# Kernel tuning notes

Measured on AMD Instinct MI355X. Metric: run time of the kernel, lower is better.

Reference implementation:

```python
import jax, jax.numpy as jnp
import numpy as np

B, T, TWO_H = 64, 512, 1024  # batch, prev decoding steps, 2*hidden_dim


def setup_inputs() -> dict:
    key = jax.random.key(0)
    k1, k2, k3 = jax.random.split(key, 3)
    h_d_t = jax.random.normal(k1, (B, TWO_H), dtype=jnp.float32)
    prev_h_dec = jax.random.normal(k2, (B, T, TWO_H), dtype=jnp.float32)
    # nn.Bilinear(2H, 2H, attn_dim=1) weight, trunc_norm_init_std ~ 1e-4 typical
    W = jax.random.normal(k3, (1, TWO_H, TWO_H), dtype=jnp.float32) * 1e-4
    return {"h_d_t": h_d_t, "prev_h_dec": prev_h_dec, "W": W}


def reference(h_d_t, prev_h_dec, W):
    # Bilinear score: s[b,t] = h_d_t[b] @ W[0] @ prev_h_dec[b,t]
    q = jnp.einsum('bd,de->be', h_d_t, W[0])          # (B, 2H) -- one small GEMM
    attn_score = jnp.einsum('be,bte->bt', q, prev_h_dec)  # (B, T)
    alpha_t = jax.nn.softmax(attn_score, axis=1)      # (B, T)
    ct_d = jnp.einsum('bt,btd->bd', alpha_t, prev_h_dec)  # (B, 2H)
    new_prev = jnp.concatenate([prev_h_dec, h_d_t[:, None, :]], axis=1)  # (B, T+1, 2H)
    return (ct_d, new_prev)
```

## Files before the change

kernel.cpp:

```cpp
#include <hip/hip_runtime.h>
#include <math.h>

#define BB    64
#define TT    512
#define TWOH  1024
#define TC    16
#define NCHUNK (TT / TC)
#define KSPLIT 4
#define NP_STRIDE ((TT + 1) * TWOH)

typedef float vfloat4 __attribute__((ext_vector_type(4)));


__global__ __launch_bounds__(256) void k_qgemm(const float* __restrict__ h,
                                               const float* __restrict__ W,
                                               float* __restrict__ qpart) {
    const int tid = threadIdx.x;
    const int e   = blockIdx.x * 256 + tid;
    const int b   = blockIdx.y;
    const int k   = blockIdx.z;
    const int d0  = k * (TWOH / KSPLIT);

    __shared__ float sh[TWOH / KSPLIT];
    sh[tid] = h[b * TWOH + d0 + tid];
    __syncthreads();

    const float* __restrict__ Wp = W + (size_t)d0 * TWOH + e;
    float acc = 0.f;
    #pragma unroll 16
    for (int d = 0; d < TWOH / KSPLIT; ++d)
        acc = fmaf(sh[d], Wp[(size_t)d * TWOH], acc);

    qpart[((size_t)k * BB + b) * TWOH + e] = acc;
}

__global__ __launch_bounds__(256, 4) void k_scores_ct(const float* __restrict__ prev,
                                                      const float* __restrict__ qpart,
                                                      float* __restrict__ out_np,
                                                      float* __restrict__ ws_m,
                                                      float* __restrict__ ws_l,
                                                      float* __restrict__ ws_ct) {
    const int c   = blockIdx.x;
    const int b   = blockIdx.y;
    const int t0  = c * TC;
    const int tid = threadIdx.x;
    const int lane = tid & 63;
    const int wid  = tid >> 6;

    __shared__ float s_part[TC][4];
    __shared__ float s_score[TC];

    const vfloat4* __restrict__ prow =
        (const vfloat4*)(prev + (size_t)b * TT * TWOH + (size_t)t0 * TWOH) + tid;
    vfloat4* __restrict__ nprow =
        (vfloat4*)(out_np + (size_t)b * NP_STRIDE + (size_t)t0 * TWOH) + tid;

    const vfloat4* __restrict__ qp = (const vfloat4*)qpart;
    vfloat4 q4 = qp[((size_t)0 * BB + b) * 256 + tid]
               + qp[((size_t)1 * BB + b) * 256 + tid]
               + qp[((size_t)2 * BB + b) * 256 + tid]
               + qp[((size_t)3 * BB + b) * 256 + tid];

    vfloat4 pv[TC];
    #pragma unroll
    for (int t = 0; t < TC; ++t)
        pv[t] = prow[t * 256];

    #pragma unroll
    for (int t = 0; t < TC; ++t) {
        float pd = pv[t].x * q4.x + pv[t].y * q4.y + pv[t].z * q4.z + pv[t].w * q4.w;
        #pragma unroll
        for (int off = 32; off > 0; off >>= 1)
            pd += __shfl_xor(pd, off, 64);
        if (lane == 0) s_part[t][wid] = pd;
    }
    __syncthreads();
    if (tid < TC)
        s_score[tid] = s_part[tid][0] + s_part[tid][1] + s_part[tid][2] + s_part[tid][3];
    __syncthreads();

    float m = -INFINITY;
    #pragma unroll
    for (int t = 0; t < TC; ++t) m = fmaxf(m, s_score[t]);
    float l = 0.f;
    vfloat4 ct = (vfloat4)(0.f);
    #pragma unroll
    for (int t = 0; t < TC; ++t) {
        const float w = __expf(s_score[t] - m);
        l += w;
        ct.x = fmaf(w, pv[t].x, ct.x);
        ct.y = fmaf(w, pv[t].y, ct.y);
        ct.z = fmaf(w, pv[t].z, ct.z);
        ct.w = fmaf(w, pv[t].w, ct.w);
    }
    ((vfloat4*)(ws_ct + ((size_t)b * NCHUNK + c) * TWOH))[tid] = ct;
    if (tid == 0) {
        ws_m[b * NCHUNK + c] = m;
        ws_l[b * NCHUNK + c] = l;
    }

    #pragma unroll
    for (int t = 0; t < TC; ++t)
        nprow[t * 256] = pv[t];
}

__global__ __launch_bounds__(256) void k_finalize(const float* __restrict__ h,
                                                  const float* __restrict__ ws_m,
                                                  const float* __restrict__ ws_l,
                                                  const float* __restrict__ ws_ct,
                                                  float* __restrict__ out_ct,
                                                  float* __restrict__ out_np) {
    const int tid = threadIdx.x;
    const int e   = blockIdx.x * 256 + tid;
    const int b   = blockIdx.y;

    float M = -INFINITY;
    #pragma unroll
    for (int i = 0; i < NCHUNK; ++i) M = fmaxf(M, ws_m[b * NCHUNK + i]);

    float coef[NCHUNK];
    float L = 0.f;
    #pragma unroll
    for (int i = 0; i < NCHUNK; ++i) {
        const float ce = __expf(ws_m[b * NCHUNK + i] - M);
        coef[i] = ce;
        L = fmaf(ce, ws_l[b * NCHUNK + i], L);
    }
    const float inv = 1.0f / L;

    const float* __restrict__ cp = ws_ct + (size_t)b * NCHUNK * TWOH + e;
    float acc = 0.f;
    #pragma unroll
    for (int i = 0; i < NCHUNK; ++i)
        acc = fmaf(coef[i], cp[(size_t)i * TWOH], acc);
    out_ct[b * TWOH + e] = acc * inv;

    out_np[(size_t)b * NP_STRIDE + (size_t)TT * TWOH + e] = h[b * TWOH + e];
}

extern "C" void kernel_launch(void* const* d_in, const int* in_sizes, int n_in,
                              void* d_out, int out_size, void* d_ws, size_t ws_size,
                              hipStream_t stream) {
    const float* h    = (const float*)d_in[0];
    const float* prev = (const float*)d_in[1];
    const float* W    = (const float*)d_in[2];
    float* out    = (float*)d_out;
    float* out_ct = out;
    float* out_np = out + BB * TWOH;

    float* qpart = (float*)d_ws;
    float* wsm   = qpart + KSPLIT * BB * TWOH;
    float* wsl   = wsm + BB * NCHUNK;
    float* wsc   = wsl + BB * NCHUNK;

    k_qgemm<<<dim3(4, BB, KSPLIT), 256, 0, stream>>>(h, W, qpart);
    k_scores_ct<<<dim3(NCHUNK, BB), 256, 0, stream>>>(prev, qpart, out_np, wsm, wsl, wsc);
    k_finalize<<<dim3(4, BB), 256, 0, stream>>>(h, wsm, wsl, wsc, out_ct, out_np);
}
```

Before: 266.6 us.

## Assign rows per wavefront with online softmax and register prefetch

Restructures the score/context kernel so each wavefront owns 8 full rows and processes them one at a time, using an online softmax with a one-row register prefetch. This removes block-level __syncthreads and shared-memory reductions and cuts the register footprint from 16 rows per thread. In exchange it doubles the number of partial context vectors (64 groups per batch) written to workspace and read back by the finalize kernel, which also now recomputes exp per chunk.

Result: no change. 267.6 us (+0.4%).

```diff
diff --git a/kernel.cpp b/kernel.cpp
--- a/kernel.cpp
+++ b/kernel.cpp
@@ -4,8 +4,9 @@
 #define BB    64
 #define TT    512
 #define TWOH  1024
-#define TC    16
-#define NCHUNK (TT / TC)
+#define RPW   8
+#define WPB   4
+#define NG    (TT / RPW)
 #define KSPLIT 4
 #define NP_STRIDE ((TT + 1) * TWOH)
 
@@ -40,68 +41,87 @@
                                                       float* __restrict__ ws_m,
                                                       float* __restrict__ ws_l,
                                                       float* __restrict__ ws_ct) {
-    const int c   = blockIdx.x;
-    const int b   = blockIdx.y;
-    const int t0  = c * TC;
-    const int tid = threadIdx.x;
+    const int tid  = threadIdx.x;
     const int lane = tid & 63;
     const int wid  = tid >> 6;
+    const int b    = blockIdx.y;
+    const int g    = blockIdx.x * WPB + wid;
+    const int t0   = g * RPW;
 
-    __shared__ float s_part[TC][4];
-    __shared__ float s_score[TC];
+    const vfloat4* __restrict__ qp = (const vfloat4*)qpart;
+    const int qb0 = ((0 * BB + b) * 256) + lane;
+    const int qb1 = ((1 * BB + b) * 256) + lane;
+    const int qb2 = ((2 * BB + b) * 256) + lane;
+    const int qb3 = ((3 * BB + b) * 256) + lane;
+    vfloat4 q0 = qp[qb0      ] + qp[qb1      ] + qp[qb2      ] + qp[qb3      ];
+    vfloat4 q1 = qp[qb0 +  64] + qp[qb1 +  64] + qp[qb2 +  64] + qp[qb3 +  64];
+    vfloat4 q2 = qp[qb0 + 128] + qp[qb1 + 128] + qp[qb2 + 128] + qp[qb3 + 128];
+    vfloat4 q3 = qp[qb0 + 192] + qp[qb1 + 192] + qp[qb2 + 192] + qp[qb3 + 192];
 
     const vfloat4* __restrict__ prow =
-        (const vfloat4*)(prev + (size_t)b * TT * TWOH + (size_t)t0 * TWOH) + tid;
+        (const vfloat4*)(prev + ((size_t)b * TT + (size_t)t0) * TWOH) + lane;
     vfloat4* __restrict__ nprow =
-        (vfloat4*)(out_np + (size_t)b * NP_STRIDE + (size_t)t0 * TWOH) + tid;
+        (vfloat4*)(out_np + (size_t)b * NP_STRIDE + (size_t)t0 * TWOH) + lane;
 
-    const vfloat4* __restrict__ qp = (const vfloat4*)qpart;
-    vfloat4 q4 = qp[((size_t)0 * BB + b) * 256 + tid]
-               + qp[((size_t)1 * BB + b) * 256 + tid]
-               + qp[((size_t)2 * BB + b) * 256 + tid]
-               + qp[((size_t)3 * BB + b) * 256 + tid];
+    vfloat4 c0 = prow[0], c1 = prow[64], c2 = prow[128], c3 = prow[192];
 
-    vfloat4 pv[TC];
-    #pragma unroll
-    for (int t = 0; t < TC; ++t)
-        pv[t] = prow[t * 256];
+    float m = -INFINITY;
+    float l = 0.f;
+    vfloat4 ct0 = (vfloat4)(0.f), ct1 = (vfloat4)(0.f),
+            ct2 = (vfloat4)(0.f), ct3 = (vfloat4)(0.f);
 
     #pragma unroll
-    for (int t = 0; t < TC; ++t) {
-        float pd = pv[t].x * q4.x + pv[t].y * q4.y + pv[t].z * q4.z + pv[t].w * q4.w;
+    for (int r = 0; r < RPW; ++r) {
+        vfloat4 n0, n1, n2, n3;
+        if (r + 1 < RPW) {
+            const int o = (r + 1) * 256;
+            n0 = prow[o]; n1 = prow[o + 64]; n2 = prow[o + 128]; n3 = prow[o + 192];
+        }
+
+        const int so = r * 256;
+        nprow[so] = c0; nprow[so + 64] = c1; nprow[so + 128] = c2; nprow[so + 192] = c3;
+
+        float d0 = c0.x * q0.x; d0 = fmaf(c0.y, q0.y, d0);
+        d0 = fmaf(c0.z, q0.z, d0); d0 = fmaf(c0.w, q0.w, d0);
+        float d1 = c1.x * q1.x; d1 = fmaf(c1.y, q1.y, d1);
+        d1 = fmaf(c1.z, q1.z, d1); d1 = fmaf(c1.w, q1.w, d1);
+        float d2 = c2.x * q2.x; d2 = fmaf(c2.y, q2.y, d2);
+        d2 = fmaf(c2.z, q2.z, d2); d2 = fmaf(c2.w, q2.w, d2);
+        float d3 = c3.x * q3.x; d3 = fmaf(c3.y, q3.y, d3);
+        d3 = fmaf(c3.z, q3.z, d3); d3 = fmaf(c3.w, q3.w, d3);
+        float pd = (d0 + d1) + (d2 + d3);
+
         #pragma unroll
         for (int off = 32; off > 0; off >>= 1)
             pd += __shfl_xor(pd, off, 64);
-        if (lane == 0) s_part[t][wid] = pd;
-    }
-    __syncthreads();
-    if (tid < TC)
-        s_score[tid] = s_part[tid][0] + s_part[tid][1] + s_part[tid][2] + s_part[tid][3];
-    __syncthreads();
 
-    float m = -INFINITY;
-    #pragma unroll
-    for (int t = 0; t < TC; ++t) m = fmaxf(m, s_score[t]);
-    float l = 0.f;
-    vfloat4 ct = (vfloat4)(0.f);
-    #pragma unroll
-    for (int t = 0; t < TC; ++t) {
-        const float w = __expf(s_score[t] - m);
-        l += w;
-        ct.x = fmaf(w, pv[t].x, ct.x);
-        ct.y = fmaf(w, pv[t].y, ct.y);
-        ct.z = fmaf(w, pv[t].z, ct.z);
-        ct.w = fmaf(w, pv[t].w, ct.w);
-    }
-    ((vfloat4*)(ws_ct + ((size_t)b * NCHUNK + c) * TWOH))[tid] = ct;
-    if (tid == 0) {
-        ws_m[b * NCHUNK + c] = m;
-        ws_l[b * NCHUNK + c] = l;
+        if (pd > m) {
+            const float s = __expf(m - pd);
+            l *= s;
+            ct0 = ct0 * s; ct1 = ct1 * s; ct2 = ct2 * s; ct3 = ct3 * s;
+            m = pd;
+        }
+        const float a = __expf(pd - m);
+        l += a;
+        ct0.x = fmaf(a, c0.x, ct0.x); ct0.y = fmaf(a, c0.y, ct0.y);
+        ct0.z = fmaf(a, c0.z, ct0.z); ct0.w = fmaf(a, c0.w, ct0.w);
+        ct1.x = fmaf(a, c1.x, ct1.x); ct1.y = fmaf(a, c1.y, ct1.y);
+        ct1.z = fmaf(a, c1.z, ct1.z); ct1.w = fmaf(a, c1.w, ct1.w);
+        ct2.x = fmaf(a, c2.x, ct2.x); ct2.y = fmaf(a, c2.y, ct2.y);
+        ct2.z = fmaf(a, c2.z, ct2.z); ct2.w = fmaf(a, c2.w, ct2.w);
+        ct3.x = fmaf(a, c3.x, ct3.x); ct3.y = fmaf(a, c3.y, ct3.y);
+        ct3.z = fmaf(a, c3.z, ct3.z); ct3.w = fmaf(a, c3.w, ct3.w);
+
+        if (r + 1 < RPW) { c0 = n0; c1 = n1; c2 = n2; c3 = n3; }
     }
 
-    #pragma unroll
-    for (int t = 0; t < TC; ++t)
-        nprow[t * 256] = pv[t];
+    const size_t wsb = (size_t)b * NG + g;
+    vfloat4* __restrict__ wc = (vfloat4*)ws_ct + wsb * 256 + lane;
+    wc[0] = ct0; wc[64] = ct1; wc[128] = ct2; wc[192] = ct3;
+    if (lane == 0) {
+        ws_m[wsb] = m;
+        ws_l[wsb] = l;
+    }
 }
 
 __global__ __launch_bounds__(256) void k_finalize(const float* __restrict__ h,
@@ -114,25 +134,23 @@
     const int e   = blockIdx.x * 256 + tid;
     const int b   = blockIdx.y;
 
+    const float* __restrict__ wm = ws_m + b * NG;
+    const float* __restrict__ wl = ws_l + b * NG;
+
     float M = -INFINITY;
     #pragma unroll
-    for (int i = 0; i < NCHUNK; ++i) M = fmaxf(M, ws_m[b * NCHUNK + i]);
+    for (int i = 0; i < NG; ++i) M = fmaxf(M, wm[i]);
 
-    float coef[NCHUNK];
     float L = 0.f;
     #pragma unroll
-    for (int i = 0; i < NCHUNK; ++i) {
-        const float ce = __expf(ws_m[b * NCHUNK + i] - M);
-        coef[i] = ce;
-        L = fmaf(ce, ws_l[b * NCHUNK + i], L);
-    }
+    for (int i = 0; i < NG; ++i) L = fmaf(__expf(wm[i] - M), wl[i], L);
     const float inv = 1.0f / L;
 
-    const float* __restrict__ cp = ws_ct + (size_t)b * NCHUNK * TWOH + e;
+    const float* __restrict__ cp = ws_ct + (size_t)b * NG * TWOH + e;
     float acc = 0.f;
     #pragma unroll
-    for (int i = 0; i < NCHUNK; ++i)
-        acc = fmaf(coef[i], cp[(size_t)i * TWOH], acc);
+    for (int i = 0; i < NG; ++i)
+        acc = fmaf(__expf(wm[i] - M), cp[(size_t)i * TWOH], acc);
     out_ct[b * TWOH + e] = acc * inv;
 
     out_np[(size_t)b * NP_STRIDE + (size_t)TT * TWOH + e] = h[b * TWOH + e];
@@ -150,10 +168,10 @@
 
     float* qpart = (float*)d_ws;
     float* wsm   = qpart + KSPLIT * BB * TWOH;
-    float* wsl   = wsm + BB * NCHUNK;
-    float* wsc   = wsl + BB * NCHUNK;
+    float* wsl   = wsm + BB * NG;
+    float* wsc   = wsl + BB * NG;
 
     k_qgemm<<<dim3(4, BB, KSPLIT), 256, 0, stream>>>(h, W, qpart);
-    k_scores_ct<<<dim3(NCHUNK, BB), 256, 0, stream>>>(prev, qpart, out_np, wsm, wsl, wsc);
+    k_scores_ct<<<dim3(NG / WPB, BB), 256, 0, stream>>>(prev, qpart, out_np, wsm, wsl, wsc);
     k_finalize<<<dim3(4, BB), 256, 0, stream>>>(h, wsm, wsl, wsc, out_ct, out_np);
 }
```

## Give each wavefront its own rows with per-wave softmax, merged once in LDS

Applied to the files above, without the earlier changes.

Restructures the scores/context kernel so each 64-lane wavefront owns 4 full rows and reduces each dot product with shuffles only. The cross-wave score exchange and its two barriers are replaced by a per-wave online-softmax partial, merged once through shared memory. The new_prev copy-out is also issued right after the loads rather than at the end. This adds 16 KB of LDS per block and an extra merge step, which could lower occupancy.

Result: no change. 262.1 us (-1.7%).

```diff
diff --git a/kernel.cpp b/kernel.cpp
--- a/kernel.cpp
+++ b/kernel.cpp
@@ -4,7 +4,9 @@
 #define BB    64
 #define TT    512
 #define TWOH  1024
-#define TC    16
+#define RPW   4
+#define WPB   4
+#define TC    (RPW * WPB)
 #define NCHUNK (TT / TC)
 #define KSPLIT 4
 #define NP_STRIDE ((TT + 1) * TWOH)
@@ -40,68 +42,120 @@
                                                       float* __restrict__ ws_m,
                                                       float* __restrict__ ws_l,
                                                       float* __restrict__ ws_ct) {
-    const int c   = blockIdx.x;
-    const int b   = blockIdx.y;
-    const int t0  = c * TC;
-    const int tid = threadIdx.x;
+    const int tid  = threadIdx.x;
     const int lane = tid & 63;
     const int wid  = tid >> 6;
-
-    __shared__ float s_part[TC][4];
-    __shared__ float s_score[TC];
+    const int c    = blockIdx.x;
+    const int b    = blockIdx.y;
+    const int t0   = c * TC + wid * RPW;
+
+    __shared__ float s_ct[WPB][TWOH];
+    __shared__ float s_m[WPB];
+    __shared__ float s_l[WPB];
+
+    const vfloat4* __restrict__ qp = (const vfloat4*)qpart;
+    vfloat4 q[4];
+    #pragma unroll
+    for (int j = 0; j < 4; ++j)
+        q[j] = qp[(0 * BB + b) * 256 + j * 64 + lane]
+             + qp[(1 * BB + b) * 256 + j * 64 + lane]
+             + qp[(2 * BB + b) * 256 + j * 64 + lane]
+             + qp[(3 * BB + b) * 256 + j * 64 + lane];
 
     const vfloat4* __restrict__ prow =
-        (const vfloat4*)(prev + (size_t)b * TT * TWOH + (size_t)t0 * TWOH) + tid;
+        (const vfloat4*)(prev + ((size_t)b * TT + (size_t)t0) * TWOH) + lane;
     vfloat4* __restrict__ nprow =
-        (vfloat4*)(out_np + (size_t)b * NP_STRIDE + (size_t)t0 * TWOH) + tid;
-
-    const vfloat4* __restrict__ qp = (const vfloat4*)qpart;
-    vfloat4 q4 = qp[((size_t)0 * BB + b) * 256 + tid]
-               + qp[((size_t)1 * BB + b) * 256 + tid]
-               + qp[((size_t)2 * BB + b) * 256 + tid]
-               + qp[((size_t)3 * BB + b) * 256 + tid];
-
-    vfloat4 pv[TC];
-    #pragma unroll
-    for (int t = 0; t < TC; ++t)
-        pv[t] = prow[t * 256];
-
-    #pragma unroll
-    for (int t = 0; t < TC; ++t) {
-        float pd = pv[t].x * q4.x + pv[t].y * q4.y + pv[t].z * q4.z + pv[t].w * q4.w;
+        (vfloat4*)(out_np + (size_t)b * NP_STRIDE + (size_t)t0 * TWOH) + lane;
+
+    vfloat4 cv[RPW][4];
+    #pragma unroll
+    for (int r = 0; r < RPW; ++r)
+        #pragma unroll
+        for (int j = 0; j < 4; ++j)
+            cv[r][j] = prow[r * 256 + j * 64];
+
+    #pragma unroll
+    for (int r = 0; r < RPW; ++r)
+        #pragma unroll
+        for (int j = 0; j < 4; ++j)
+            nprow[r * 256 + j * 64] = cv[r][j];
+
+    float pd[RPW];
+    #pragma unroll
+    for (int r = 0; r < RPW; ++r) {
+        float d0 = cv[r][0].x * q[0].x;
+        d0 = fmaf(cv[r][0].y, q[0].y, d0);
+        d0 = fmaf(cv[r][0].z, q[0].z, d0);
+        d0 = fmaf(cv[r][0].w, q[0].w, d0);
+        float d1 = cv[r][1].x * q[1].x;
+        d1 = fmaf(cv[r][1].y, q[1].y, d1);
+        d1 = fmaf(cv[r][1].z, q[1].z, d1);
+        d1 = fmaf(cv[r][1].w, q[1].w, d1);
+        float d2 = cv[r][2].x * q[2].x;
+        d2 = fmaf(cv[r][2].y, q[2].y, d2);
+        d2 = fmaf(cv[r][2].z, q[2].z, d2);
+        d2 = fmaf(cv[r][2].w, q[2].w, d2);
+        float d3 = cv[r][3].x * q[3].x;
+        d3 = fmaf(cv[r][3].y, q[3].y, d3);
+        d3 = fmaf(cv[r][3].z, q[3].z, d3);
+        d3 = fmaf(cv[r][3].w, q[3].w, d3);
+        pd[r] = (d0 + d1) + (d2 + d3);
+    }
+    #pragma unroll
+    for (int r = 0; r < RPW; ++r)
         #pragma unroll
         for (int off = 32; off > 0; off >>= 1)
-            pd += __shfl_xor(pd, off, 64);
-        if (lane == 0) s_part[t][wid] = pd;
-    }
+            pd[r] += __shfl_xor(pd[r], off, 64);
+
+    const float m = fmaxf(fmaxf(pd[0], pd[1]), fmaxf(pd[2], pd[3]));
+    float a[RPW];
+    float l = 0.f;
+    #pragma unroll
+    for (int r = 0; r < RPW; ++r) {
+        a[r] = __expf(pd[r] - m);
+        l += a[r];
+    }
+    vfloat4 ct[4];
+    #pragma unroll
+    for (int j = 0; j < 4; ++j) ct[j] = (vfloat4)(0.f);
+    #pragma unroll
+    for (int r = 0; r < RPW; ++r)
+        #pragma unroll
+        for (int j = 0; j < 4; ++j) {
+            ct[j].x = fmaf(a[r], cv[r][j].x, ct[j].x);
+            ct[j].y = fmaf(a[r], cv[r][j].y, ct[j].y);
+            ct[j].z = fmaf(a[r], cv[r][j].z, ct[j].z);
+            ct[j].w = fmaf(a[r], cv[r][j].w, ct[j].w);
+        }
+
+    vfloat4* __restrict__ sct = (vfloat4*)&s_ct[wid][0];
+    #pragma unroll
+    for (int j = 0; j < 4; ++j) sct[j * 64 + lane] = ct[j];
+    if (lane == 0) { s_m[wid] = m; s_l[wid] = l; }
     __syncthreads();
-    if (tid < TC)
-        s_score[tid] = s_part[tid][0] + s_part[tid][1] + s_part[tid][2] + s_part[tid][3];
-    __syncthreads();
-
-    float m = -INFINITY;
-    #pragma unroll
-    for (int t = 0; t < TC; ++t) m = fmaxf(m, s_score[t]);
-    float l = 0.f;
-    vfloat4 ct = (vfloat4)(0.f);
-    #pragma unroll
-    for (int t = 0; t < TC; ++t) {
-        const float w = __expf(s_score[t] - m);
-        l += w;
-        ct.x = fmaf(w, pv[t].x, ct.x);
-        ct.y = fmaf(w, pv[t].y, ct.y);
-        ct.z = fmaf(w, pv[t].z, ct.z);
-        ct.w = fmaf(w, pv[t].w, ct.w);
-    }
-    ((vfloat4*)(ws_ct + ((size_t)b * NCHUNK + c) * TWOH))[tid] = ct;
+
+    const float M = fmaxf(fmaxf(s_m[0], s_m[1]), fmaxf(s_m[2], s_m[3]));
+    float L = 0.f;
+    float co[WPB];
+    #pragma unroll
+    for (int w = 0; w < WPB; ++w) {
+        co[w] = __expf(s_m[w] - M);
+        L = fmaf(co[w], s_l[w], L);
+    }
+    vfloat4 o = (vfloat4)(0.f);
+    #pragma unroll
+    for (int w = 0; w < WPB; ++w) {
+        const vfloat4 v = ((const vfloat4*)&s_ct[w][0])[tid];
+        o.x = fmaf(co[w], v.x, o.x);
+        o.y = fmaf(co[w], v.y, o.y);
+        o.z = fmaf(co[w], v.z, o.z);
+        o.w = fmaf(co[w], v.w, o.w);
+    }
+    ((vfloat4*)(ws_ct + ((size_t)b * NCHUNK + c) * TWOH))[tid] = o;
     if (tid == 0) {
-        ws_m[b * NCHUNK + c] = m;
-        ws_l[b * NCHUNK + c] = l;
-    }
-
-    #pragma unroll
-    for (int t = 0; t < TC; ++t)
-        nprow[t * 256] = pv[t];
+        ws_m[b * NCHUNK + c] = M;
+        ws_l[b * NCHUNK + c] = L;
+    }
 }
 
 __global__ __launch_bounds__(256) void k_finalize(const float* __restrict__ h,
@@ -114,26 +168,23 @@
     const int e   = blockIdx.x * 256 + tid;
     const int b   = blockIdx.y;
 
+    const float* __restrict__ wm = ws_m + b * NCHUNK;
+    const float* __restrict__ wl = ws_l + b * NCHUNK;
+
     float M = -INFINITY;
     #pragma unroll
-    for (int i = 0; i < NCHUNK; ++i) M = fmaxf(M, ws_m[b * NCHUNK + i]);
-
-    float coef[NCHUNK];
+    for (int i = 0; i < NCHUNK; ++i) M = fmaxf(M, wm[i]);
+
+    const float* __restrict__ cp = ws_ct + (size_t)b * NCHUNK * TWOH + e;
     float L = 0.f;
+    float acc = 0.f;
     #pragma unroll
     for (int i = 0; i < NCHUNK; ++i) {
-        const float ce = __expf(ws_m[b * NCHUNK + i] - M);
-        coef[i] = ce;
-        L = fmaf(ce, ws_l[b * NCHUNK + i], L);
-    }
-    const float inv = 1.0f / L;
-
-    const float* __restrict__ cp = ws_ct + (size_t)b * NCHUNK * TWOH + e;
-    float acc = 0.f;
-    #pragma unroll
-    for (int i = 0; i < NCHUNK; ++i)
-        acc = fmaf(coef[i], cp[(size_t)i * TWOH], acc);
-    out_ct[b * TWOH + e] = acc * inv;
+        const float ce = __expf(wm[i] - M);
+        L   = fmaf(ce, wl[i], L);
+        acc = fmaf(ce, cp[(size_t)i * TWOH], acc);
+    }
+    out_ct[b * TWOH + e] = acc * (1.0f / L);
 
     out_np[(size_t)b * NP_STRIDE + (size_t)TT * TWOH + e] = h[b * TWOH + e];
 }
```

## Stage prev rows via global_load_lds with one wave per timestep

Applied to the files above, without the earlier changes.

Restructures the score/context kernel so each block handles 4 timesteps, one wave per row. Rows are loaded directly into LDS with global_load_lds, then copied to the output and reused from LDS for the dot product and the weighted sum. The q partial-sum reduction moves into its own small kernel, and the finalize loop is streamlined. The aim is lower register pressure, higher occupancy and more blocks to hide memory latency. In exchange the chunk count rises fourfold, which enlarges the ws_ct partial-context workspace that finalize must read back, and adds one more kernel launch.

New measurement: 276.5 us. 3.7% more time.

```diff
diff --git a/kernel.cpp b/kernel.cpp
--- a/kernel.cpp
+++ b/kernel.cpp
@@ -4,13 +4,21 @@
 #define BB    64
 #define TT    512
 #define TWOH  1024
-#define TC    16
-#define NCHUNK (TT / TC)
+#define WPB   4
+#define TCB   WPB
+#define NCHUNK (TT / TCB)
 #define KSPLIT 4
 #define NP_STRIDE ((TT + 1) * TWOH)
 
 typedef float vfloat4 __attribute__((ext_vector_type(4)));
 
+
+__device__ __forceinline__ void gload_lds16(const float* g, float* l) {
+    __builtin_amdgcn_global_load_lds(
+        (const __attribute__((address_space(1))) unsigned int*)g,
+        (__attribute__((address_space(3))) unsigned int*)l,
+        16, 0, 0);
+}
 
 __global__ __launch_bounds__(256) void k_qgemm(const float* __restrict__ h,
                                                const float* __restrict__ W,
@@ -34,74 +42,96 @@
     qpart[((size_t)k * BB + b) * TWOH + e] = acc;
 }
 
-__global__ __launch_bounds__(256, 4) void k_scores_ct(const float* __restrict__ prev,
-                                                      const float* __restrict__ qpart,
+__global__ __launch_bounds__(256) void k_qreduce(const float* __restrict__ qpart,
+                                                 float* __restrict__ q) {
+    const int b   = blockIdx.x;
+    const int tid = threadIdx.x;
+    const vfloat4* __restrict__ qp = (const vfloat4*)qpart;
+    const vfloat4 s = qp[(0 * BB + b) * 256 + tid]
+                    + qp[(1 * BB + b) * 256 + tid]
+                    + qp[(2 * BB + b) * 256 + tid]
+                    + qp[(3 * BB + b) * 256 + tid];
+    ((vfloat4*)(q + (size_t)b * TWOH))[tid] = s;
+}
+
+__global__ __launch_bounds__(256, 8) void k_scores_ct(const float* __restrict__ prev,
+                                                      const float* __restrict__ q,
                                                       float* __restrict__ out_np,
                                                       float* __restrict__ ws_m,
                                                       float* __restrict__ ws_l,
                                                       float* __restrict__ ws_ct) {
-    const int c   = blockIdx.x;
-    const int b   = blockIdx.y;
-    const int t0  = c * TC;
-    const int tid = threadIdx.x;
+    const int tid  = threadIdx.x;
     const int lane = tid & 63;
     const int wid  = tid >> 6;
+    const int c    = blockIdx.x;
+    const int b    = blockIdx.y;
+    const int t    = c * TCB + wid;
 
-    __shared__ float s_part[TC][4];
-    __shared__ float s_score[TC];
+    __shared__ float srow[WPB][TWOH];
+    __shared__ float sscore[WPB];
 
-    const vfloat4* __restrict__ prow =
-        (const vfloat4*)(prev + (size_t)b * TT * TWOH + (size_t)t0 * TWOH) + tid;
+    const float* gbase = prev + ((size_t)b * TT + t) * TWOH;
+    #pragma unroll
+    for (int j = 0; j < 4; ++j)
+        gload_lds16(gbase + j * 256 + lane * 4, &srow[wid][j * 256]);
+
+    const vfloat4* __restrict__ qv = (const vfloat4*)(q + (size_t)b * TWOH);
+    const vfloat4 q0 = qv[lane];
+    const vfloat4 q1 = qv[64 + lane];
+    const vfloat4 q2 = qv[128 + lane];
+    const vfloat4 q3 = qv[192 + lane];
+
+    asm volatile("s_waitcnt vmcnt(0)" ::: "memory");
+    __builtin_amdgcn_sched_barrier(0);
+
+    const vfloat4* sr = (const vfloat4*)&srow[wid][0];
     vfloat4* __restrict__ nprow =
-        (vfloat4*)(out_np + (size_t)b * NP_STRIDE + (size_t)t0 * TWOH) + tid;
-
-    const vfloat4* __restrict__ qp = (const vfloat4*)qpart;
-    vfloat4 q4 = qp[((size_t)0 * BB + b) * 256 + tid]
-               + qp[((size_t)1 * BB + b) * 256 + tid]
-               + qp[((size_t)2 * BB + b) * 256 + tid]
-               + qp[((size_t)3 * BB + b) * 256 + tid];
-
-    vfloat4 pv[TC];
+        (vfloat4*)(out_np + (size_t)b * NP_STRIDE + (size_t)t * TWOH) + lane;
+    const vfloat4 v0 = sr[lane];
+    const vfloat4 v1 = sr[64 + lane];
+    const vfloat4 v2 = sr[128 + lane];
+    const vfloat4 v3 = sr[192 + lane];
+    nprow[0]   = v0;
+    nprow[64]  = v1;
+    nprow[128] = v2;
+    nprow[192] = v3;
+    float d0 = v0.x * q0.x; d0 = fmaf(v0.y, q0.y, d0);
+    d0 = fmaf(v0.z, q0.z, d0); d0 = fmaf(v0.w, q0.w, d0);
+    float d1 = v1.x * q1.x; d1 = fmaf(v1.y, q1.y, d1);
+    d1 = fmaf(v1.z, q1.z, d1); d1 = fmaf(v1.w, q1.w, d1);
+    float d2 = v2.x * q2.x; d2 = fmaf(v2.y, q2.y, d2);
+    d2 = fmaf(v2.z, q2.z, d2); d2 = fmaf(v2.w, q2.w, d2);
+    float d3 = v3.x * q3.x; d3 = fmaf(v3.y, q3.y, d3);
+    d3 = fmaf(v3.z, q3.z, d3); d3 = fmaf(v3.w, q3.w, d3);
+    float pd = (d0 + d1) + (d2 + d3);
     #pragma unroll
-    for (int t = 0; t < TC; ++t)
-        pv[t] = prow[t * 256];
-
-    #pragma unroll
-    for (int t = 0; t < TC; ++t) {
-        float pd = pv[t].x * q4.x + pv[t].y * q4.y + pv[t].z * q4.z + pv[t].w * q4.w;
-        #pragma unroll
-        for (int off = 32; off > 0; off >>= 1)
-            pd += __shfl_xor(pd, off, 64);
-        if (lane == 0) s_part[t][wid] = pd;
-    }
-    __syncthreads();
-    if (tid < TC)
-        s_score[tid] = s_part[tid][0] + s_part[tid][1] + s_part[tid][2] + s_part[tid][3];
+    for (int off = 32; off > 0; off >>= 1)
+        pd += __shfl_xor(pd, off, 64);
+    if (lane == 0) sscore[wid] = pd;
     __syncthreads();
 
-    float m = -INFINITY;
-    #pragma unroll
-    for (int t = 0; t < TC; ++t) m = fmaxf(m, s_score[t]);
-    float l = 0.f;
-    vfloat4 ct = (vfloat4)(0.f);
-    #pragma unroll
-    for (int t = 0; t < TC; ++t) {
-        const float w = __expf(s_score[t] - m);
-        l += w;
-        ct.x = fmaf(w, pv[t].x, ct.x);
-        ct.y = fmaf(w, pv[t].y, ct.y);
-        ct.z = fmaf(w, pv[t].z, ct.z);
-        ct.w = fmaf(w, pv[t].w, ct.w);
+    const float s0 = sscore[0], s1 = sscore[1], s2 = sscore[2], s3 = sscore[3];
+    const float M  = fmaxf(fmaxf(s0, s1), fmaxf(s2, s3));
+    const float a0 = __expf(s0 - M);
+    const float a1 = __expf(s1 - M);
+    const float a2 = __expf(s2 - M);
+    const float a3 = __expf(s3 - M);
+    const float L  = (a0 + a1) + (a2 + a3);
+
+    const vfloat4 x0 = ((const vfloat4*)&srow[0][0])[tid];
+    const vfloat4 x1 = ((const vfloat4*)&srow[1][0])[tid];
+    const vfloat4 x2 = ((const vfloat4*)&srow[2][0])[tid];
+    const vfloat4 x3 = ((const vfloat4*)&srow[3][0])[tid];
+    vfloat4 o;
+    o.x = fmaf(a3, x3.x, fmaf(a2, x2.x, fmaf(a1, x1.x, a0 * x0.x)));
+    o.y = fmaf(a3, x3.y, fmaf(a2, x2.y, fmaf(a1, x1.y, a0 * x0.y)));
+    o.z = fmaf(a3, x3.z, fmaf(a2, x2.z, fmaf(a1, x1.z, a0 * x0.z)));
+    o.w = fmaf(a3, x3.w, fmaf(a2, x2.w, fmaf(a1, x1.w, a0 * x0.w)));
+    ((vfloat4*)(ws_ct + ((size_t)b * NCHUNK + c) * TWOH))[tid] = o;
+    if (tid == 0) {
+        ws_m[b * NCHUNK + c] = M;
+        ws_l[b * NCHUNK + c] = L;
     }
-    ((vfloat4*)(ws_ct + ((size_t)b * NCHUNK + c) * TWOH))[tid] = ct;
-    if (tid == 0) {
-        ws_m[b * NCHUNK + c] = m;
-        ws_l[b * NCHUNK + c] = l;
-    }
-
-    #pragma unroll
-    for (int t = 0; t < TC; ++t)
-        nprow[t * 256] = pv[t];
 }
 
 __global__ __launch_bounds__(256) void k_finalize(const float* __restrict__ h,
@@ -114,26 +144,23 @@
     const int e   = blockIdx.x * 256 + tid;
     const int b   = blockIdx.y;
 
+    const float* __restrict__ wm = ws_m + b * NCHUNK;
+    const float* __restrict__ wl = ws_l + b * NCHUNK;
+
     float M = -INFINITY;
-    #pragma unroll
-    for (int i = 0; i < NCHUNK; ++i) M = fmaxf(M, ws_m[b * NCHUNK + i]);
-
-    float coef[NCHUNK];
-    float L = 0.f;
-    #pragma unroll
-    for (int i = 0; i < NCHUNK; ++i) {
-        const float ce = __expf(ws_m[b * NCHUNK + i] - M);
-        coef[i] = ce;
-        L = fmaf(ce, ws_l[b * NCHUNK + i], L);
-    }
-    const float inv = 1.0f / L;
+    #pragma unroll 32
+    for (int i = 0; i < NCHUNK; ++i) M = fmaxf(M, wm[i]);
 
     const float* __restrict__ cp = ws_ct + (size_t)b * NCHUNK * TWOH + e;
+    float L = 0.f;
     float acc = 0.f;
-    #pragma unroll
-    for (int i = 0; i < NCHUNK; ++i)
-        acc = fmaf(coef[i], cp[(size_t)i * TWOH], acc);
-    out_ct[b * TWOH + e] = acc * inv;
+    #pragma unroll 32
+    for (int i = 0; i < NCHUNK; ++i) {
+        const float ce = __expf(wm[i] - M);
+        L   = fmaf(ce, wl[i], L);
+        acc = fmaf(ce, cp[(size_t)i * TWOH], acc);
+    }
+    out_ct[b * TWOH + e] = acc * (1.0f / L);
 
     out_np[(size_t)b * NP_STRIDE + (size_t)TT * TWOH + e] = h[b * TWOH + e];
 }
@@ -149,11 +176,13 @@
     float* out_np = out + BB * TWOH;
 
     float* qpart = (float*)d_ws;
-    float* wsm   = qpart + KSPLIT * BB * TWOH;
+    float* qred  = qpart + KSPLIT * BB * TWOH;
+    float* wsm   = qred + BB * TWOH;
     float* wsl   = wsm + BB * NCHUNK;
     float* wsc   = wsl + BB * NCHUNK;
 
     k_qgemm<<<dim3(4, BB, KSPLIT), 256, 0, stream>>>(h, W, qpart);
-    k_scores_ct<<<dim3(NCHUNK, BB), 256, 0, stream>>>(prev, qpart, out_np, wsm, wsl, wsc);
+    k_qreduce<<<dim3(BB), 256, 0, stream>>>(qpart, qred);
+    k_scores_ct<<<dim3(NCHUNK, BB), 256, 0, stream>>>(prev, qred, out_np, wsm, wsl, wsc);
     k_finalize<<<dim3(4, BB), 256, 0, stream>>>(h, wsm, wsl, wsc, out_ct, out_np);
 }
```
